# Kernel optimization log

Hardware: AMD Instinct MI355X
Metric: run time of the kernel (lower is better)

The kernel has to match this reference:

```python
import jax, jax.numpy as jnp
from jax import lax
import numpy as np

B, DIM, HEADS, L, K = 8, 128, 8, 4096, 3
INNER = DIM * HEADS
PAD = K // 2
EPS = 1e-5
SCALE = DIM ** -0.5


def setup_inputs() -> dict:
    key = jax.random.key(0)
    ks = jax.random.split(key, 32)

    def n(i, shape, s):
        return jax.random.normal(ks[i], shape, jnp.float32) * s

    inp = {"x": jax.random.normal(ks[0], (B, DIM, L), jnp.float32)}
    inp["ln1_g"] = jnp.ones((DIM,), jnp.float32)
    inp["ln1_b"] = jnp.zeros((DIM,), jnp.float32)
    for idx, p in enumerate(("q", "k", "v")):
        base = 1 + idx * 2
        inp[p + "_dw"] = n(base, (DIM, 1, K), 0.2)        # depthwise kernel
        inp[p + "_bn_g"] = jnp.ones((DIM,), jnp.float32)
        inp[p + "_bn_b"] = jnp.zeros((DIM,), jnp.float32)
        inp[p + "_bn_m"] = jnp.zeros((DIM,), jnp.float32)  # running mean
        inp[p + "_bn_v"] = jnp.ones((DIM,), jnp.float32)   # running var
        inp[p + "_pw"] = n(base + 1, (INNER, DIM), 0.05)   # 1x1 conv dim->inner
    inp["dwc_dw"] = n(8, (DIM,), 0.2)                      # kernel-1 depthwise = per-channel scale
    inp["dwc_bn_g"] = jnp.ones((DIM,), jnp.float32)
    inp["dwc_bn_b"] = jnp.zeros((DIM,), jnp.float32)
    inp["dwc_bn_m"] = jnp.zeros((DIM,), jnp.float32)
    inp["dwc_bn_v"] = jnp.ones((DIM,), jnp.float32)
    inp["dwc_pw"] = n(9, (DIM, DIM), 0.05)
    inp["out_w"] = n(10, (DIM, INNER), 0.05)
    inp["out_b"] = jnp.zeros((DIM,), jnp.float32)
    inp["ln2_g"] = jnp.ones((DIM,), jnp.float32)
    inp["ln2_b"] = jnp.zeros((DIM,), jnp.float32)
    inp["ff_w1"] = n(11, (4 * DIM, DIM), 0.05)
    inp["ff_b1"] = jnp.zeros((4 * DIM,), jnp.float32)
    inp["ff_w2"] = n(12, (DIM, 4 * DIM), 0.05)
    inp["ff_b2"] = jnp.zeros((DIM,), jnp.float32)
    return inp


def _layernorm(x, g, b):
    # channel-wise LN over axis=1 (unbiased=False variance)
    m = jnp.mean(x, axis=1, keepdims=True)
    v = jnp.var(x, axis=1, keepdims=True)
    return (x - m) / jnp.sqrt(v + EPS) * g[None, :, None] + b[None, :, None]


def _dw_block(x, dw, g, b, m, v, pw):
    # depthwise conv (k=K, same padding) -> eval-mode BN -> 1x1 conv
    y = lax.conv_general_dilated(x, dw, (1,), [(PAD, PAD)],
                                 feature_group_count=DIM,
                                 dimension_numbers=("NCH", "OIH", "NCH"))
    y = (y - m[None, :, None]) * (g / jnp.sqrt(v + EPS))[None, :, None] + b[None, :, None]
    return jnp.einsum("oi,bil->bol", pw, y)


def reference(x, ln1_g, ln1_b,
              q_dw, q_bn_g, q_bn_b, q_bn_m, q_bn_v, q_pw,
              k_dw, k_bn_g, k_bn_b, k_bn_m, k_bn_v, k_pw,
              v_dw, v_bn_g, v_bn_b, v_bn_m, v_bn_v, v_pw,
              dwc_dw, dwc_bn_g, dwc_bn_b, dwc_bn_m, dwc_bn_v, dwc_pw,
              out_w, out_b, ln2_g, ln2_b, ff_w1, ff_b1, ff_w2, ff_b2):
    # ---- attention block (PreNorm + residual) ----
    xn = _layernorm(x, ln1_g, ln1_b)
    q = _dw_block(xn, q_dw, q_bn_g, q_bn_b, q_bn_m, q_bn_v, q_pw)  # [B, INNER, L]
    k = _dw_block(xn, k_dw, k_bn_g, k_bn_b, k_bn_m, k_bn_v, k_pw)
    v = _dw_block(xn, v_dw, v_bn_g, v_bn_b, v_bn_m, v_bn_v, v_pw)

    def split(t):  # b (h d) x -> (b h) x d
        return t.reshape(B, HEADS, DIM, L).transpose(0, 1, 3, 2).reshape(B * HEADS, L, DIM)

    q, k, v = split(q), split(k), split(v)
    k_soft = jax.nn.softmax(k, axis=-1)                       # softmax over feature dim d
    kk = jnp.einsum("nxd,nxe->nde", q, k_soft) * SCALE        # [(bh), d, d]
    # DWConv gate on q (kernel-1 depthwise -> BN -> 1x1), channels = DIM
    g_ = q * dwc_dw[None, None, :]
    g_ = (g_ - dwc_bn_m) * (dwc_bn_g / jnp.sqrt(dwc_bn_v + EPS)) + dwc_bn_b
    g_ = jnp.einsum("od,nxd->nxo", dwc_pw, g_)
    gate = jax.nn.sigmoid(g_) * v
    out = jnp.einsum("nxd,nde->nxe", v, kk) + gate            # [(bh), L, d]
    out = out.reshape(B, HEADS, L, DIM).transpose(0, 1, 3, 2).reshape(B, INNER, L)
    attn = jnp.einsum("oi,bil->bol", out_w, out) + out_b[None, :, None]
    x = attn + x

    # ---- feed-forward block (PreNorm + residual) ----
    xn = _layernorm(x, ln2_g, ln2_b)
    h = jnp.einsum("oi,bil->bol", ff_w1, xn) + ff_b1[None, :, None]
    h = jax.nn.gelu(h, approximate=False)
    h = jnp.einsum("oi,bil->bol", ff_w2, h) + ff_b2[None, :, None]
    return h + x
```

## Files before the change

kernel.cpp:

```cpp
#include <hip/hip_runtime.h>
#include <hip/hip_bf16.h>
#include <math.h>

#define DI __device__ __forceinline__

namespace {

constexpr int L = 4096;
constexpr float EPS = 1e-5f;
constexpr float SCALEF = 0.08838834764831845f;

typedef unsigned short u16;
typedef unsigned int u32;
typedef unsigned char u8;
typedef __attribute__((ext_vector_type(8))) short bf16x8;
typedef __attribute__((ext_vector_type(4))) float f32x4;

DI float b2f(u16 h){ u32 u = ((u32)h) << 16; float f; __builtin_memcpy(&f, &u, 4); return f; }
DI u16 f2b(float f){ u32 u; __builtin_memcpy(&u, &f, 4); u32 r = u + 0x7fffu + ((u >> 16) & 1u); return (u16)(r >> 16); }
DI float sigmoidf(float x){ return 1.f / (1.f + __expf(-x)); }

DI uint2 pack_fp8x8(const float* v){
  u32 lo = __builtin_amdgcn_cvt_pk_fp8_f32(v[0], v[1], 0, false);
  lo = (u32)__builtin_amdgcn_cvt_pk_fp8_f32(v[2], v[3], lo, true);
  u32 hi = __builtin_amdgcn_cvt_pk_fp8_f32(v[4], v[5], 0, false);
  hi = (u32)__builtin_amdgcn_cvt_pk_fp8_f32(v[6], v[7], hi, true);
  return make_uint2(lo, hi);
}
DI u8 f2e(float v){ return (u8)__builtin_amdgcn_cvt_pk_fp8_f32(v, v, 0, false); }
DI float e2f(u8 c){ return __builtin_amdgcn_cvt_f32_fp8((int)c, 0); }

DI int boff(int o, int d8){ return ((o >> 4) << 11) + (d8 << 7) + (((o & 15) ^ d8) << 3); }
DI int foff(int g, int k8, int nn){ return (g << 11) + (k8 << 7) + (nn << 3); }
DI int faddr(int x, int e){ return ((x >> 4) << 11) + ((e >> 3) << 7) + ((x & 15) << 3) + (e & 7); }
DI int t8off(int dhi, int nl, int x8){ return (dhi << 11) + (x8 << 7) + (((nl ^ x8 ^ dhi) & 15) << 3); }

DI void stage_a(const u16* __restrict__ g, int rs, u16* a_s, int tid){
  #pragma unroll
  for (int it = 0; it < 4; it++){
    int item = tid + 256 * it;
    int d8 = item & 15, l = item >> 4;
    *(uint4*)&a_s[l * 136 + d8 * 8] = *(const uint4*)&g[(size_t)l * rs + d8 * 8];
  }
}

__global__ __launch_bounds__(256) void ln_kernel(
    const float* __restrict__ x, const float* __restrict__ g,
    const float* __restrict__ bt, u16* __restrict__ o)
{
  const int tid = threadIdx.x;
  const int pos = blockIdx.x * 64 + (tid >> 2);
  const int part = tid & 3;
  const int b = pos >> 12, l = pos & (L - 1);
  const float* xb = x + (size_t)b * 128 * L + l;
  float vv[32];
  float s = 0.f, ss = 0.f;
  #pragma unroll
  for (int i = 0; i < 32; i++){
    float v = xb[(size_t)(part * 32 + i) * L];
    vv[i] = v; s += v; ss += v * v;
  }
  s += __shfl_xor(s, 1);  s += __shfl_xor(s, 2);
  ss += __shfl_xor(ss, 1); ss += __shfl_xor(ss, 2);
  const float m = s * (1.f / 128.f);
  const float rs = rsqrtf(ss * (1.f / 128.f) - m * m + EPS);
  #pragma unroll
  for (int c = 0; c < 4; c++){
    u16 pk[8];
    #pragma unroll
    for (int j = 0; j < 8; j++){
      int d = part * 32 + c * 8 + j;
      pk[j] = f2b((vv[c * 8 + j] - m) * rs * g[d] + bt[d]);
    }
    uint4 uu; __builtin_memcpy(&uu, pk, 16);
    *(uint4*)&o[(size_t)pos * 128 + part * 32 + c * 8] = uu;
  }
}

__global__ __launch_bounds__(256) void wpack_kernel(
    const float* __restrict__ q_pw, const float* __restrict__ k_pw,
    const float* __restrict__ v_pw, const float* __restrict__ out_w,
    const float* __restrict__ ff_w1, const float* __restrict__ ff_w2,
    const float* __restrict__ dwc_dw, const float* __restrict__ dwc_bng,
    const float* __restrict__ dwc_bnb, const float* __restrict__ dwc_bnm,
    const float* __restrict__ dwc_bnv, const float* __restrict__ dwc_pw,
    u16* __restrict__ wpk, u8* __restrict__ w2tb8, float* __restrict__ c2,
    u8* __restrict__ wpk8)
{
  const int blk = blockIdx.x;
  if (blk < 320){
    int item = blk * 256 + threadIdx.x;
    int d8 = item & 15;
    int o  = (item >> 4) & 127;
    int t  = item >> 11;
    const float* src;
    if (t < 24){
      int p = t >> 3, h = t & 7;
      const float* pw = (p == 0) ? q_pw : (p == 1 ? k_pw : v_pw);
      src = pw + (size_t)(h * 128 + o) * 128 + d8 * 8;
    } else if (t < 32){
      src = out_w + (size_t)o * 1024 + (t - 24) * 128 + d8 * 8;
    } else if (t < 36){
      src = ff_w1 + (size_t)((t - 32) * 128 + o) * 128 + d8 * 8;
    } else {
      src = ff_w2 + (size_t)o * 512 + (t - 36) * 128 + d8 * 8;
    }
    u16 pk[8];
    #pragma unroll
    for (int j = 0; j < 8; j++) pk[j] = f2b(src[j]);
    uint4 uu; __builtin_memcpy(&uu, pk, 16);
    *(uint4*)&wpk[(size_t)t * 16384 + boff(o, d8)] = uu;
  } else if (blk == 320){
    #pragma unroll
    for (int it = 0; it < 8; it++){
      int item = threadIdx.x + 256 * it;
      int nn = item & 15, k8 = (item >> 4) & 15, os = item >> 8;
      int e = os * 16 + nn;
      float fv[8];
      #pragma unroll
      for (int j = 0; j < 8; j++){
        int d = k8 * 8 + j;
        float sD = dwc_bng[d] * rsqrtf(dwc_bnv[d] + EPS);
        fv[j] = dwc_pw[(size_t)e * 128 + d] * dwc_dw[d] * sD * 16.f;
      }
      *(uint2*)&w2tb8[foff(os, k8, nn)] = pack_fp8x8(fv);
    }
  } else if (blk == 321){
    int e = threadIdx.x;
    if (e < 128){
      float cacc = 0.f;
      for (int d = 0; d < 128; d++){
        float sD = dwc_bng[d] * rsqrtf(dwc_bnv[d] + EPS);
        cacc += dwc_pw[(size_t)e * 128 + d] * (dwc_bnb[d] - dwc_bnm[d] * sD);
      }
      c2[e] = cacc;
    }
  } else {
    int h = blk - 322;
    #pragma unroll
    for (int it = 0; it < 8; it++){
      int item = threadIdx.x + 256 * it;
      int nn = item & 15, k8 = (item >> 4) & 15, os = item >> 8;
      int o = os * 16 + nn;
      float fv[8];
      #pragma unroll
      for (int j = 0; j < 8; j++)
        fv[j] = out_w[(size_t)o * 1024 + h * 128 + k8 * 8 + j] * 16.f;
      *(uint2*)&wpk8[(h << 14) + foff(os, k8, nn)] = pack_fp8x8(fv);
    }
  }
}

struct QkvArgs {
  const float* dw[3];
  const float* bng[3];
  const float* bnb[3];
  const float* bnm[3];
  const float* bnv[3];
  u8* outp[3];
};

__global__ __launch_bounds__(256, 3) void qkv_fused_kernel(
    const u16* __restrict__ xnb, const u16* __restrict__ wpk, QkvArgs args)
{
  __shared__ u16 y_s[64 * 136];
  __shared__ u16 w_s[128 * 128];
  __shared__ float4 coef[128];
  const int tid = threadIdx.x;
  const int lb = blockIdx.x;
  const int oh = blockIdx.y;
  const int bz = blockIdx.z;
  const int b  = bz / 3;
  const int p  = bz % 3;
  const int l0 = lb * 64;
  const int lane = tid & 63, wv = tid >> 6;
  const int nn = lane & 15, quad = lane >> 4;
  const int d8s = tid & 15;

  if (tid < 128){
    int d = tid;
    float sD = args.bng[p][d] * rsqrtf(args.bnv[p][d] + EPS);
    const float* dw = args.dw[p];
    coef[d] = make_float4(dw[d * 3] * sD, dw[d * 3 + 1] * sD, dw[d * 3 + 2] * sD,
                          args.bnb[p][d] - args.bnm[p][d] * sD);
  }
  __syncthreads();
  float4 cf[8];
  #pragma unroll
  for (int jj = 0; jj < 8; jj++) cf[jj] = coef[d8s * 8 + jj];
  #pragma unroll
  for (int it = 0; it < 4; it++){
    int l = (tid >> 4) + it * 16;
    int gl = l0 + l;
    const u16* rowp = xnb + ((size_t)b * L + gl) * 128 + d8s * 8;
    uint4 uc = *(const uint4*)rowp;
    uint4 um = (gl > 0)     ? *(const uint4*)(rowp - 128) : make_uint4(0, 0, 0, 0);
    uint4 up = (gl < L - 1) ? *(const uint4*)(rowp + 128) : make_uint4(0, 0, 0, 0);
    u16 em[8], ec[8], ep[8];
    __builtin_memcpy(em, &um, 16); __builtin_memcpy(ec, &uc, 16); __builtin_memcpy(ep, &up, 16);
    u16 pk[8];
    #pragma unroll
    for (int jj = 0; jj < 8; jj++)
      pk[jj] = f2b(cf[jj].x * b2f(em[jj]) + cf[jj].y * b2f(ec[jj]) + cf[jj].z * b2f(ep[jj]) + cf[jj].w);
    uint4 uu; __builtin_memcpy(&uu, pk, 16);
    *(uint4*)&y_s[l * 136 + d8s * 8] = uu;
  }
  __syncthreads();
  bf16x8 af[4];
  #pragma unroll
  for (int dc = 0; dc < 4; dc++)
    af[dc] = *(const bf16x8*)&y_s[(wv * 16 + nn) * 136 + ((dc << 2) + quad) * 8];

  for (int hh = 0; hh < 4; hh++){
    const int h = oh * 4 + hh;
    const int ph = p * 8 + h;
    if (hh) __syncthreads();
    const u16* src = wpk + ((size_t)ph << 14);
    #pragma unroll
    for (int it = 0; it < 8; it++){
      int idx = (tid + 256 * it) << 3;
      *(uint4*)&w_s[idx] = *(const uint4*)&src[idx];
    }
    __syncthreads();
    f32x4 acc[8];
    #pragma unroll
    for (int os = 0; os < 8; os++) acc[os] = (f32x4){0.f, 0.f, 0.f, 0.f};
    #pragma unroll
    for (int os = 0; os < 8; os++){
      #pragma unroll
      for (int dc = 0; dc < 4; dc++){
        int d8 = (dc << 2) + quad;
        bf16x8 bf = *(const bf16x8*)&w_s[(os << 11) + (d8 << 7) + ((nn ^ d8) << 3)];
        acc[os] = __builtin_amdgcn_mfma_f32_16x16x32_bf16(af[dc], bf, acc[os], 0, 0, 0);
      }
    }
    if (p == 1){
      #pragma unroll
      for (int r = 0; r < 4; r++){
        float m = acc[0][r];
        #pragma unroll
        for (int os = 1; os < 8; os++) m = fmaxf(m, acc[os][r]);
        m = fmaxf(m, __shfl_xor(m, 1));
        m = fmaxf(m, __shfl_xor(m, 2));
        m = fmaxf(m, __shfl_xor(m, 4));
        m = fmaxf(m, __shfl_xor(m, 8));
        float s = 0.f;
        #pragma unroll
        for (int os = 0; os < 8; os++){ acc[os][r] = __expf(acc[os][r] - m); s += acc[os][r]; }
        s += __shfl_xor(s, 1);
        s += __shfl_xor(s, 2);
        s += __shfl_xor(s, 4);
        s += __shfl_xor(s, 8);
        float inv = 16.f / s;
        #pragma unroll
        for (int os = 0; os < 8; os++) acc[os][r] *= inv;
      }
    }
    __syncthreads();
    u16* st = w_s;
    #pragma unroll
    for (int os = 0; os < 8; os++)
      #pragma unroll
      for (int r = 0; r < 4; r++)
        st[(wv * 16 + quad * 4 + r) * 136 + (os << 4) + nn] = f2b(acc[os][r]);
    __syncthreads();
    if (p == 2){
      u8* v8 = args.outp[2];
      size_t tbase = ((size_t)((b * 8 + h) * 64 + lb)) << 13;
      #pragma unroll
      for (int it = 0; it < 4; it++){
        int g = it, e8 = tid >> 4, n2 = tid & 15;
        const u16* sp = &st[(g * 16 + n2) * 136 + e8 * 8];
        float fv[8];
        #pragma unroll
        for (int j = 0; j < 8; j++) fv[j] = b2f(sp[j]);
        *(uint2*)&v8[tbase + foff(g, e8, n2)] = pack_fp8x8(fv);
      }
    } else {
      u8* outp8 = args.outp[p];
      size_t gbase = ((size_t)(b * 8 + h) * L + l0) * 128;
      #pragma unroll
      for (int it = 0; it < 4; it++){
        int item = tid + 256 * it;
        int row = item >> 4, d8 = item & 15;
        const u16* sp = &st[row * 136 + d8 * 8];
        float fv[8];
        #pragma unroll
        for (int j = 0; j < 8; j++) fv[j] = b2f(sp[j]);
        *(uint2*)&outp8[gbase + (size_t)row * 128 + d8 * 8] = pack_fp8x8(fv);
      }
    }
  }
}

__global__ __launch_bounds__(256, 3) void kk_kernel(
    const u8* __restrict__ qt8, const u8* __restrict__ kt8,
    float* __restrict__ kkp)
{
  __shared__ u8 qT8[16384];
  __shared__ u8 kT8[16384];
  const int tid = threadIdx.x;
  const int sp = blockIdx.x;
  const int n  = blockIdx.y;
  const int d8 = tid & 15;
  const int x8 = tid >> 4;
  const int lane = tid & 63, wv = tid >> 6;
  const int nn = lane & 15, quad = lane >> 4;
  const int m4 = (wv >> 1) << 2;
  const int e4 = (wv & 1) << 2;
  const size_t gbase = ((size_t)n * L + sp * 1024) * 128;

  uint2 rq[8], rk[8];
  #pragma unroll
  for (int j = 0; j < 8; j++){
    size_t off = gbase + (size_t)(x8 * 8 + j) * 128 + d8 * 8;
    rq[j] = *(const uint2*)&qt8[off];
    rk[j] = *(const uint2*)&kt8[off];
  }

  f32x4 acc[4][4];
  #pragma unroll
  for (int mi = 0; mi < 4; mi++)
    #pragma unroll
    for (int ei = 0; ei < 4; ei++) acc[mi][ei] = (f32x4){0.f, 0.f, 0.f, 0.f};

  for (int c = 0; c < 8; c++){
    #pragma unroll
    for (int i = 0; i < 8; i++){
      u8 cq[8], ck[8];
      #pragma unroll
      for (int j = 0; j < 8; j++){
        u8 tmp[8];
        __builtin_memcpy(tmp, &rq[j], 8); cq[j] = tmp[i];
        __builtin_memcpy(tmp, &rk[j], 8); ck[j] = tmp[i];
      }
      int d = d8 * 8 + i;
      int off = t8off(d >> 4, d & 15, x8);
      uint2 uq, uk;
      __builtin_memcpy(&uq, cq, 8); __builtin_memcpy(&uk, ck, 8);
      *(uint2*)&qT8[off] = uq;
      *(uint2*)&kT8[off] = uk;
    }
    __syncthreads();
    if (c < 7){
      #pragma unroll
      for (int j = 0; j < 8; j++){
        size_t off = gbase + (size_t)((c + 1) * 128 + x8 * 8 + j) * 128 + d8 * 8;
        rq[j] = *(const uint2*)&qt8[off];
        rk[j] = *(const uint2*)&kt8[off];
      }
    }
    #pragma unroll
    for (int ks = 0; ks < 4; ks++){
      int x8f = (ks << 2) + quad;
      long af[4], bf[4];
      #pragma unroll
      for (int t = 0; t < 4; t++){
        af[t] = *(const long*)&qT8[t8off(m4 + t, nn, x8f)];
        bf[t] = *(const long*)&kT8[t8off(e4 + t, nn, x8f)];
      }
      #pragma unroll
      for (int mi = 0; mi < 4; mi++)
        #pragma unroll
        for (int ei = 0; ei < 4; ei++)
          acc[mi][ei] = __builtin_amdgcn_mfma_f32_16x16x32_fp8_fp8(af[mi], bf[ei], acc[mi][ei], 0, 0, 0);
    }
    __syncthreads();
  }

  float* op = kkp + ((size_t)(sp * 64 + n) << 14);
  #pragma unroll
  for (int mi = 0; mi < 4; mi++){
    #pragma unroll
    for (int r = 0; r < 4; r++){
      int d = (m4 << 4) + mi * 16 + quad * 4 + r;
      #pragma unroll
      for (int ei = 0; ei < 4; ei++)
        op[d * 128 + (e4 << 4) + ei * 16 + nn] = acc[mi][ei][r];
    }
  }
}

__global__ __launch_bounds__(256) void kkred_kernel(
    const float* __restrict__ kkp, u8* __restrict__ kkbb8)
{
  int item = blockIdx.x * 256 + threadIdx.x;
  int nn = item & 15, d8 = (item >> 4) & 15, os = (item >> 8) & 7, n = item >> 11;
  int e = os * 16 + nn;
  float fv[8];
  #pragma unroll
  for (int j = 0; j < 8; j++){
    float s = 0.f;
    #pragma unroll
    for (int sp = 0; sp < 4; sp++)
      s += kkp[(size_t)sp * (64 * 16384) + n * 16384 + (d8 * 8 + j) * 128 + e];
    fv[j] = s * (SCALEF * 2.f);
  }
  *(uint2*)&kkbb8[((size_t)n << 14) + foff(os, d8, nn)] = pack_fp8x8(fv);
}

__global__ __launch_bounds__(256, 4) void gateout_kernel(
    const u8* __restrict__ qt8, const u8* __restrict__ vt8,
    const u8* __restrict__ kkbb8, const u8* __restrict__ w2tb8,
    const float* __restrict__ c2, u8* __restrict__ outt8)
{
  __shared__ __attribute__((aligned(16))) u8 q_s8[64 * 144];
  __shared__ __attribute__((aligned(16))) u8 v_s8[8192];
  const int tid = threadIdx.x;
  const int lb = blockIdx.x;
  const int n  = blockIdx.y;
  const int l0 = lb * 64;
  const int lane = tid & 63, wv = tid >> 6;
  const int nn = lane & 15, quad = lane >> 4;
  const size_t vtile = ((size_t)(n * 64 + lb)) << 13;
  const size_t qbase = ((size_t)n * L + l0) * 128;

  #pragma unroll
  for (int it = 0; it < 4; it++){
    int item = tid + 256 * it;
    int d8b = item & 15, l = item >> 4;
    *(uint2*)&q_s8[l * 144 + d8b * 8] = *(const uint2*)&qt8[qbase + (size_t)l * 128 + d8b * 8];
  }
  #pragma unroll
  for (int it = 0; it < 2; it++){
    int idx = (tid + 256 * it) << 4;
    *(uint4*)&v_s8[idx] = *(const uint4*)&vt8[vtile + idx];
  }
  __syncthreads();

  long aq[4], av[4];
  #pragma unroll
  for (int dc = 0; dc < 4; dc++){
    aq[dc] = *(const long*)&q_s8[(wv * 16 + nn) * 144 + ((dc << 2) + quad) * 8];
    av[dc] = *(const long*)&v_s8[foff(wv, (dc << 2) + quad, nn)];
  }
  const u8* kb8 = kkbb8 + ((size_t)n << 14);
  f32x4 acc_o[8], acc_g[8];
  #pragma unroll
  for (int os = 0; os < 8; os++){ acc_o[os] = (f32x4){0,0,0,0}; acc_g[os] = (f32x4){0,0,0,0}; }
  #pragma unroll
  for (int os = 0; os < 8; os++){
    #pragma unroll
    for (int dc = 0; dc < 4; dc++){
      int d8 = (dc << 2) + quad;
      long bkk = *(const long*)&kb8[foff(os, d8, nn)];
      long bw8 = *(const long*)&w2tb8[foff(os, d8, nn)];
      acc_o[os] = __builtin_amdgcn_mfma_f32_16x16x32_fp8_fp8(av[dc], bkk, acc_o[os], 0, 0, 0);
      acc_g[os] = __builtin_amdgcn_mfma_f32_16x16x32_fp8_fp8(aq[dc], bw8, acc_g[os], 0, 0, 0);
    }
  }
  __syncthreads();
  u8* st8 = q_s8;
  #pragma unroll
  for (int os = 0; os < 8; os++){
    int e = (os << 4) + nn;
    float c2v = c2[e];
    #pragma unroll
    for (int r = 0; r < 4; r++){
      int xr = wv * 16 + quad * 4 + r;
      float ve = e2f(v_s8[faddr(xr, e)]);
      float val = acc_o[os][r] * (1.f / 32.f) + sigmoidf(acc_g[os][r] * 0.0625f + c2v) * ve;
      st8[faddr(xr, e)] = f2e(val);
    }
  }
  __syncthreads();
  #pragma unroll
  for (int it = 0; it < 2; it++){
    int idx = (tid + 256 * it) << 4;
    *(uint4*)&outt8[vtile + idx] = *(const uint4*)&st8[idx];
  }
}

__global__ __launch_bounds__(256, 4) void outw_kernel(
    const u8* __restrict__ outt8, const u8* __restrict__ wpk8,
    const float* __restrict__ out_b, const float* __restrict__ x,
    const float* __restrict__ g2, const float* __restrict__ bt2,
    float* __restrict__ x2, u16* __restrict__ xn2b)
{
  __shared__ float stf[128 * 68];
  const int tid = threadIdx.x;
  const int lb = blockIdx.x;
  const int b  = blockIdx.y;
  const int l0 = lb * 64;
  const int lane = tid & 63, wv = tid >> 6;
  const int nn = lane & 15, quad = lane >> 4;
  f32x4 acc[8];
  #pragma unroll
  for (int os = 0; os < 8; os++) acc[os] = (f32x4){0,0,0,0};

  for (int h = 0; h < 8; h++){
    const size_t tbase = ((size_t)((b * 8 + h) * 64 + lb)) << 13;
    long af[4];
    #pragma unroll
    for (int dc = 0; dc < 4; dc++)
      af[dc] = *(const long*)&outt8[tbase + foff(wv, (dc << 2) + quad, nn)];
    const u8* bp8 = wpk8 + (h << 14);
    #pragma unroll
    for (int os = 0; os < 8; os++){
      #pragma unroll
      for (int dc = 0; dc < 4; dc++){
        long bf8 = *(const long*)&bp8[foff(os, (dc << 2) + quad, nn)];
        acc[os] = __builtin_amdgcn_mfma_f32_16x16x32_fp8_fp8(af[dc], bf8, acc[os], 0, 0, 0);
      }
    }
  }
  #pragma unroll
  for (int os = 0; os < 8; os++)
    #pragma unroll
    for (int r = 0; r < 4; r++)
      stf[((os << 4) + nn) * 68 + wv * 16 + quad * 4 + r] = acc[os][r] * 0.0625f;
  __syncthreads();
  {
    int o = tid >> 1, lh = tid & 1;
    float bias = out_b[o];
    size_t gbase = ((size_t)b * 128 + o) * L + l0 + lh * 32;
    float* sp = &stf[o * 68 + lh * 32];
    #pragma unroll
    for (int k = 0; k < 8; k++){
      float4 xv = *(const float4*)&x[gbase + k * 4];
      float4 sv = *(float4*)&sp[k * 4];
      float4 ov = make_float4(sv.x + bias + xv.x, sv.y + bias + xv.y,
                              sv.z + bias + xv.z, sv.w + bias + xv.w);
      *(float4*)&sp[k * 4] = ov;
      *(float4*)&x2[gbase + k * 4] = ov;
    }
  }
  __syncthreads();
  {
    int l = tid >> 2, part = tid & 3;
    float vv[32];
    float s = 0.f, ss = 0.f;
    #pragma unroll
    for (int i = 0; i < 32; i++){
      float v = stf[(part * 32 + i) * 68 + l];
      vv[i] = v; s += v; ss += v * v;
    }
    s += __shfl_xor(s, 1);  s += __shfl_xor(s, 2);
    ss += __shfl_xor(ss, 1); ss += __shfl_xor(ss, 2);
    float m = s * (1.f / 128.f);
    float rs = rsqrtf(ss * (1.f / 128.f) - m * m + EPS);
    #pragma unroll
    for (int c = 0; c < 4; c++){
      u16 pk[8];
      #pragma unroll
      for (int j = 0; j < 8; j++){
        int d = part * 32 + c * 8 + j;
        pk[j] = f2b((vv[c * 8 + j] - m) * rs * g2[d] + bt2[d]);
      }
      uint4 uu; __builtin_memcpy(&uu, pk, 16);
      *(uint4*)&xn2b[((size_t)b * L + l0 + l) * 128 + part * 32 + c * 8] = uu;
    }
  }
}

__global__ __launch_bounds__(256, 2) void ff_fused_kernel(
    const u16* __restrict__ xn2b, const u16* __restrict__ wpk,
    const float* __restrict__ b1, const float* __restrict__ b2,
    const float* __restrict__ x2, float* __restrict__ outp)
{
  __shared__ u16 a_s[64 * 136];
  __shared__ u16 h_s[64 * 136];
  const int tid = threadIdx.x;
  const int lb = blockIdx.x;
  const int b  = blockIdx.y;
  const int l0 = lb * 64;
  const int lane = tid & 63, wv = tid >> 6;
  const int nn = lane & 15, quad = lane >> 4;

  stage_a(xn2b + ((size_t)b * L + l0) * 128, 128, a_s, tid);
  __syncthreads();
  bf16x8 af[4];
  #pragma unroll
  for (int dc = 0; dc < 4; dc++)
    af[dc] = *(const bf16x8*)&a_s[(wv * 16 + nn) * 136 + ((dc << 2) + quad) * 8];

  f32x4 acc_out[8];
  #pragma unroll
  for (int os = 0; os < 8; os++) acc_out[os] = (f32x4){0.f, 0.f, 0.f, 0.f};

  for (int fc = 0; fc < 4; fc++){
    const u16* bp1 = wpk + (size_t)(32 + fc) * 16384;
    f32x4 hacc[8];
    #pragma unroll
    for (int os = 0; os < 8; os++) hacc[os] = (f32x4){0.f, 0.f, 0.f, 0.f};
    #pragma unroll
    for (int os = 0; os < 8; os++){
      #pragma unroll
      for (int dc = 0; dc < 4; dc++){
        int d8 = (dc << 2) + quad;
        bf16x8 bf = *(const bf16x8*)&bp1[(os << 11) + (d8 << 7) + ((nn ^ d8) << 3)];
        hacc[os] = __builtin_amdgcn_mfma_f32_16x16x32_bf16(af[dc], bf, hacc[os], 0, 0, 0);
      }
    }
    __syncthreads();
    #pragma unroll
    for (int os = 0; os < 8; os++){
      float bias = b1[fc * 128 + (os << 4) + nn];
      #pragma unroll
      for (int r = 0; r < 4; r++){
        float v = hacc[os][r] + bias;
        float ge = 0.5f * v * (1.f + erff(v * 0.70710678118654752f));
        h_s[(wv * 16 + quad * 4 + r) * 136 + (os << 4) + nn] = f2b(ge);
      }
    }
    __syncthreads();
    bf16x8 hf[4];
    #pragma unroll
    for (int dc = 0; dc < 4; dc++)
      hf[dc] = *(const bf16x8*)&h_s[(wv * 16 + nn) * 136 + ((dc << 2) + quad) * 8];
    const u16* bp2 = wpk + (size_t)(36 + fc) * 16384;
    #pragma unroll
    for (int os = 0; os < 8; os++){
      #pragma unroll
      for (int dc = 0; dc < 4; dc++){
        int d8 = (dc << 2) + quad;
        bf16x8 bf = *(const bf16x8*)&bp2[(os << 11) + (d8 << 7) + ((nn ^ d8) << 3)];
        acc_out[os] = __builtin_amdgcn_mfma_f32_16x16x32_bf16(hf[dc], bf, acc_out[os], 0, 0, 0);
      }
    }
  }

  float* stf = (float*)h_s;
  #pragma unroll
  for (int t = 0; t < 2; t++){
    __syncthreads();
    #pragma unroll
    for (int osl = 0; osl < 4; osl++){
      int os = t * 4 + osl;
      #pragma unroll
      for (int r = 0; r < 4; r++)
        stf[((osl << 4) + nn) * 68 + wv * 16 + quad * 4 + r] = acc_out[os][r];
    }
    __syncthreads();
    int ol = tid >> 2;
    int o  = t * 64 + ol;
    int lc = (tid & 3) * 16;
    float bias = b2[o];
    size_t gbase = ((size_t)b * 128 + o) * L + l0 + lc;
    #pragma unroll
    for (int k = 0; k < 4; k++){
      float4 sv = *(const float4*)&stf[ol * 68 + lc + k * 4];
      float4 xv = *(const float4*)&x2[gbase + k * 4];
      *(float4*)&outp[gbase + k * 4] = make_float4(sv.x + bias + xv.x, sv.y + bias + xv.y,
                                                   sv.z + bias + xv.z, sv.w + bias + xv.w);
    }
  }
}

}

extern "C" void kernel_launch(void* const* d_in, const int* in_sizes, int n_in,
                              void* d_out, int out_size, void* d_ws, size_t ws_size,
                              hipStream_t stream)
{
  const float* x      = (const float*)d_in[0];
  const float* ln1_g  = (const float*)d_in[1];
  const float* ln1_b  = (const float*)d_in[2];
  const float* q_dw   = (const float*)d_in[3];
  const float* q_bng  = (const float*)d_in[4];
  const float* q_bnb  = (const float*)d_in[5];
  const float* q_bnm  = (const float*)d_in[6];
  const float* q_bnv  = (const float*)d_in[7];
  const float* q_pw   = (const float*)d_in[8];
  const float* k_dw   = (const float*)d_in[9];
  const float* k_bng  = (const float*)d_in[10];
  const float* k_bnb  = (const float*)d_in[11];
  const float* k_bnm  = (const float*)d_in[12];
  const float* k_bnv  = (const float*)d_in[13];
  const float* k_pw   = (const float*)d_in[14];
  const float* v_dw   = (const float*)d_in[15];
  const float* v_bng  = (const float*)d_in[16];
  const float* v_bnb  = (const float*)d_in[17];
  const float* v_bnm  = (const float*)d_in[18];
  const float* v_bnv  = (const float*)d_in[19];
  const float* v_pw   = (const float*)d_in[20];
  const float* dwc_dw  = (const float*)d_in[21];
  const float* dwc_bng = (const float*)d_in[22];
  const float* dwc_bnb = (const float*)d_in[23];
  const float* dwc_bnm = (const float*)d_in[24];
  const float* dwc_bnv = (const float*)d_in[25];
  const float* dwc_pw  = (const float*)d_in[26];
  const float* out_w  = (const float*)d_in[27];
  const float* out_b  = (const float*)d_in[28];
  const float* ln2_g  = (const float*)d_in[29];
  const float* ln2_b  = (const float*)d_in[30];
  const float* ff_w1  = (const float*)d_in[31];
  const float* ff_b1  = (const float*)d_in[32];
  const float* ff_w2  = (const float*)d_in[33];
  const float* ff_b2  = (const float*)d_in[34];
  float* out = (float*)d_out;

  char* w = (char*)d_ws;
  u8*   qt8   = (u8*)(w);
  u8*   kt8   = (u8*)(w + (32ull  << 20));
  u8*   outt8 = (u8*)(w + (64ull  << 20));
  u8*   vt8   = (u8*)(w + (128ull << 20));
  u16*  xnb   = (u16*)(w + (192ull << 20));
  u8*   kkbb8 = (u8*)(w + (192ull << 20));
  u16*  xn2b  = (u16*)(w + (192ull << 20));
  float* kkp  = (float*)(w + (200ull << 20));
  float* x2   = kkp;
  u8*   w2tb8 = (u8*)(w + (216ull << 20));
  float* c2   = (float*)(w + (216ull << 20) + 16384);
  u16*  wpk   = (u16*)(w + (216ull << 20) + 65536);
  u8*   wpk8  = (u8*)(w + (218ull << 20));

  ln_kernel<<<512, 256, 0, stream>>>(x, ln1_g, ln1_b, xnb);
  wpack_kernel<<<330, 256, 0, stream>>>(q_pw, k_pw, v_pw, out_w, ff_w1, ff_w2,
                                        dwc_dw, dwc_bng, dwc_bnb, dwc_bnm, dwc_bnv, dwc_pw,
                                        wpk, w2tb8, c2, wpk8);

  QkvArgs qa;
  qa.dw[0] = q_dw;  qa.bng[0] = q_bng; qa.bnb[0] = q_bnb; qa.bnm[0] = q_bnm; qa.bnv[0] = q_bnv; qa.outp[0] = qt8;
  qa.dw[1] = k_dw;  qa.bng[1] = k_bng; qa.bnb[1] = k_bnb; qa.bnm[1] = k_bnm; qa.bnv[1] = k_bnv; qa.outp[1] = kt8;
  qa.dw[2] = v_dw;  qa.bng[2] = v_bng; qa.bnb[2] = v_bnb; qa.bnm[2] = v_bnm; qa.bnv[2] = v_bnv; qa.outp[2] = vt8;
  qkv_fused_kernel<<<dim3(64, 2, 24), 256, 0, stream>>>(xnb, wpk, qa);

  kk_kernel<<<dim3(4, 64), 256, 0, stream>>>(qt8, kt8, kkp);
  kkred_kernel<<<512, 256, 0, stream>>>(kkp, kkbb8);
  gateout_kernel<<<dim3(64, 64), 256, 0, stream>>>(qt8, vt8, kkbb8, w2tb8, c2, outt8);
  outw_kernel<<<dim3(64, 8), 256, 0, stream>>>(outt8, wpk8, out_b, x, ln2_g, ln2_b, x2, xn2b);

  ff_fused_kernel<<<dim3(64, 8), 256, 0, stream>>>(xn2b, wpk, ff_b1, ff_b2, x2, out);
}
```

Measured before the change: 383.3 us.

## Switch QKV projection and FF first GEMM to FP8 MFMA with unified FP8 weight pack

Converts the QKV pointwise projections and the first feed-forward GEMM from bf16 to fp8 MFMA. Activations (the depthwise-conv output and the LN2 output) are quantized to fp8, and the weights are prepacked as fp8 scaled by 16, with results rescaled by 1/16. The weight-pack kernel is restructured to emit one contiguous fp8 weight buffer, which also holds the out-projection and gate weights. Only ff_w2 stays in bf16. This halves operand bytes and LDS traffic and raises the occupancy hints, at the cost of reduced numerical accuracy from fp8 quantization.

```diff
diff --git a/kernel.cpp b/kernel.cpp
--- a/kernel.cpp
+++ b/kernel.cpp
@@ -82,51 +82,57 @@
     const float* __restrict__ v_pw, const float* __restrict__ out_w,
     const float* __restrict__ ff_w1, const float* __restrict__ ff_w2,
     const float* __restrict__ dwc_dw, const float* __restrict__ dwc_bng,
-    const float* __restrict__ dwc_bnb, const float* __restrict__ dwc_bnm,
-    const float* __restrict__ dwc_bnv, const float* __restrict__ dwc_pw,
-    u16* __restrict__ wpk, u8* __restrict__ w2tb8, float* __restrict__ c2,
-    u8* __restrict__ wpk8)
+    const float* __restrict__ dwc_bnv, const float* __restrict__ dwc_bnb,
+    const float* __restrict__ dwc_bnm, const float* __restrict__ dwc_pw,
+    u16* __restrict__ wpk, float* __restrict__ c2, u8* __restrict__ wpk8)
 {
   const int blk = blockIdx.x;
-  if (blk < 320){
-    int item = blk * 256 + threadIdx.x;
-    int d8 = item & 15;
-    int o  = (item >> 4) & 127;
-    int t  = item >> 11;
-    const float* src;
-    if (t < 24){
-      int p = t >> 3, h = t & 7;
-      const float* pw = (p == 0) ? q_pw : (p == 1 ? k_pw : v_pw);
-      src = pw + (size_t)(h * 128 + o) * 128 + d8 * 8;
-    } else if (t < 32){
-      src = out_w + (size_t)o * 1024 + (t - 24) * 128 + d8 * 8;
-    } else if (t < 36){
-      src = ff_w1 + (size_t)((t - 32) * 128 + o) * 128 + d8 * 8;
-    } else {
-      src = ff_w2 + (size_t)o * 512 + (t - 36) * 128 + d8 * 8;
-    }
+  const int tid = threadIdx.x;
+  if (blk < 37){
+    int t8 = blk;
+    #pragma unroll
+    for (int it = 0; it < 8; it++){
+      int item = tid + 256 * it;
+      int nn = item & 15, k8 = (item >> 4) & 15, os = item >> 8;
+      int o = os * 16 + nn;
+      float fv[8];
+      if (t8 < 24){
+        int p = t8 >> 3, h = t8 & 7;
+        const float* pw = (p == 0) ? q_pw : (p == 1 ? k_pw : v_pw);
+        #pragma unroll
+        for (int j = 0; j < 8; j++)
+          fv[j] = pw[(size_t)(h * 128 + o) * 128 + k8 * 8 + j] * 16.f;
+      } else if (t8 < 32){
+        #pragma unroll
+        for (int j = 0; j < 8; j++)
+          fv[j] = out_w[(size_t)o * 1024 + (t8 - 24) * 128 + k8 * 8 + j] * 16.f;
+      } else if (t8 < 36){
+        #pragma unroll
+        for (int j = 0; j < 8; j++)
+          fv[j] = ff_w1[(size_t)((t8 - 32) * 128 + o) * 128 + k8 * 8 + j] * 16.f;
+      } else {
+        #pragma unroll
+        for (int j = 0; j < 8; j++){
+          int d = k8 * 8 + j;
+          float sD = dwc_bng[d] * rsqrtf(dwc_bnv[d] + EPS);
+          fv[j] = dwc_pw[(size_t)o * 128 + d] * dwc_dw[d] * sD * 16.f;
+        }
+      }
+      *(uint2*)&wpk8[(size_t)t8 * 16384 + foff(os, k8, nn)] = pack_fp8x8(fv);
+    }
+  } else if (blk < 69){
+    int vitem = (blk - 37) * 256 + tid;
+    int d8 = vitem & 15;
+    int o  = (vitem >> 4) & 127;
+    int t  = 36 + (vitem >> 11);
+    const float* src = ff_w2 + (size_t)o * 512 + (t - 36) * 128 + d8 * 8;
     u16 pk[8];
     #pragma unroll
     for (int j = 0; j < 8; j++) pk[j] = f2b(src[j]);
     uint4 uu; __builtin_memcpy(&uu, pk, 16);
     *(uint4*)&wpk[(size_t)t * 16384 + boff(o, d8)] = uu;
-  } else if (blk == 320){
-    #pragma unroll
-    for (int it = 0; it < 8; it++){
-      int item = threadIdx.x + 256 * it;
-      int nn = item & 15, k8 = (item >> 4) & 15, os = item >> 8;
-      int e = os * 16 + nn;
-      float fv[8];
-      #pragma unroll
-      for (int j = 0; j < 8; j++){
-        int d = k8 * 8 + j;
-        float sD = dwc_bng[d] * rsqrtf(dwc_bnv[d] + EPS);
-        fv[j] = dwc_pw[(size_t)e * 128 + d] * dwc_dw[d] * sD * 16.f;
-      }
-      *(uint2*)&w2tb8[foff(os, k8, nn)] = pack_fp8x8(fv);
-    }
-  } else if (blk == 321){
-    int e = threadIdx.x;
+  } else {
+    int e = tid;
     if (e < 128){
       float cacc = 0.f;
       for (int d = 0; d < 128; d++){
@@ -134,19 +140,6 @@
         cacc += dwc_pw[(size_t)e * 128 + d] * (dwc_bnb[d] - dwc_bnm[d] * sD);
       }
       c2[e] = cacc;
-    }
-  } else {
-    int h = blk - 322;
-    #pragma unroll
-    for (int it = 0; it < 8; it++){
-      int item = threadIdx.x + 256 * it;
-      int nn = item & 15, k8 = (item >> 4) & 15, os = item >> 8;
-      int o = os * 16 + nn;
-      float fv[8];
-      #pragma unroll
-      for (int j = 0; j < 8; j++)
-        fv[j] = out_w[(size_t)o * 1024 + h * 128 + k8 * 8 + j] * 16.f;
-      *(uint2*)&wpk8[(h << 14) + foff(os, k8, nn)] = pack_fp8x8(fv);
     }
   }
 }
@@ -160,11 +153,11 @@
   u8* outp[3];
 };
 
-__global__ __launch_bounds__(256, 3) void qkv_fused_kernel(
-    const u16* __restrict__ xnb, const u16* __restrict__ wpk, QkvArgs args)
-{
-  __shared__ u16 y_s[64 * 136];
-  __shared__ u16 w_s[128 * 128];
+__global__ __launch_bounds__(256, 5) void qkv_fused_kernel(
+    const u16* __restrict__ xnb, const u8* __restrict__ wpk8, QkvArgs args)
+{
+  __shared__ __attribute__((aligned(16))) u8 y_s8[64 * 136];
+  __shared__ u16 st_s[64 * 136];
   __shared__ float4 coef[128];
   const int tid = threadIdx.x;
   const int lb = blockIdx.x;
@@ -176,6 +169,7 @@
   const int lane = tid & 63, wv = tid >> 6;
   const int nn = lane & 15, quad = lane >> 4;
   const int d8s = tid & 15;
+  u8* w_s8 = (u8*)st_s;
 
   if (tid < 128){
     int d = tid;
@@ -198,28 +192,26 @@
     uint4 up = (gl < L - 1) ? *(const uint4*)(rowp + 128) : make_uint4(0, 0, 0, 0);
     u16 em[8], ec[8], ep[8];
     __builtin_memcpy(em, &um, 16); __builtin_memcpy(ec, &uc, 16); __builtin_memcpy(ep, &up, 16);
-    u16 pk[8];
+    float fv[8];
     #pragma unroll
     for (int jj = 0; jj < 8; jj++)
-      pk[jj] = f2b(cf[jj].x * b2f(em[jj]) + cf[jj].y * b2f(ec[jj]) + cf[jj].z * b2f(ep[jj]) + cf[jj].w);
-    uint4 uu; __builtin_memcpy(&uu, pk, 16);
-    *(uint4*)&y_s[l * 136 + d8s * 8] = uu;
+      fv[jj] = cf[jj].x * b2f(em[jj]) + cf[jj].y * b2f(ec[jj]) + cf[jj].z * b2f(ep[jj]) + cf[jj].w;
+    *(uint2*)&y_s8[l * 136 + d8s * 8] = pack_fp8x8(fv);
   }
   __syncthreads();
-  bf16x8 af[4];
+  long afq[4];
   #pragma unroll
   for (int dc = 0; dc < 4; dc++)
-    af[dc] = *(const bf16x8*)&y_s[(wv * 16 + nn) * 136 + ((dc << 2) + quad) * 8];
+    afq[dc] = *(const long*)&y_s8[(wv * 16 + nn) * 136 + ((dc << 2) + quad) * 8];
 
   for (int hh = 0; hh < 4; hh++){
     const int h = oh * 4 + hh;
-    const int ph = p * 8 + h;
     if (hh) __syncthreads();
-    const u16* src = wpk + ((size_t)ph << 14);
-    #pragma unroll
-    for (int it = 0; it < 8; it++){
-      int idx = (tid + 256 * it) << 3;
-      *(uint4*)&w_s[idx] = *(const uint4*)&src[idx];
+    const u8* src = wpk8 + ((size_t)(p * 8 + h) << 14);
+    #pragma unroll
+    for (int it = 0; it < 4; it++){
+      int idx = (tid + 256 * it) << 4;
+      *(uint4*)&w_s8[idx] = *(const uint4*)&src[idx];
     }
     __syncthreads();
     f32x4 acc[8];
@@ -230,10 +222,14 @@
       #pragma unroll
       for (int dc = 0; dc < 4; dc++){
         int d8 = (dc << 2) + quad;
-        bf16x8 bf = *(const bf16x8*)&w_s[(os << 11) + (d8 << 7) + ((nn ^ d8) << 3)];
-        acc[os] = __builtin_amdgcn_mfma_f32_16x16x32_bf16(af[dc], bf, acc[os], 0, 0, 0);
-      }
-    }
+        long bf8 = *(const long*)&w_s8[foff(os, d8, nn)];
+        acc[os] = __builtin_amdgcn_mfma_f32_16x16x32_fp8_fp8(afq[dc], bf8, acc[os], 0, 0, 0);
+      }
+    }
+    #pragma unroll
+    for (int os = 0; os < 8; os++)
+      #pragma unroll
+      for (int r = 0; r < 4; r++) acc[os][r] *= 0.0625f;
     if (p == 1){
       #pragma unroll
       for (int r = 0; r < 4; r++){
@@ -257,12 +253,11 @@
       }
     }
     __syncthreads();
-    u16* st = w_s;
     #pragma unroll
     for (int os = 0; os < 8; os++)
       #pragma unroll
       for (int r = 0; r < 4; r++)
-        st[(wv * 16 + quad * 4 + r) * 136 + (os << 4) + nn] = f2b(acc[os][r]);
+        st_s[(wv * 16 + quad * 4 + r) * 136 + (os << 4) + nn] = f2b(acc[os][r]);
     __syncthreads();
     if (p == 2){
       u8* v8 = args.outp[2];
@@ -270,7 +265,7 @@
       #pragma unroll
       for (int it = 0; it < 4; it++){
         int g = it, e8 = tid >> 4, n2 = tid & 15;
-        const u16* sp = &st[(g * 16 + n2) * 136 + e8 * 8];
+        const u16* sp = &st_s[(g * 16 + n2) * 136 + e8 * 8];
         float fv[8];
         #pragma unroll
         for (int j = 0; j < 8; j++) fv[j] = b2f(sp[j]);
@@ -283,7 +278,7 @@
       for (int it = 0; it < 4; it++){
         int item = tid + 256 * it;
         int row = item >> 4, d8 = item & 15;
-        const u16* sp = &st[row * 136 + d8 * 8];
+        const u16* sp = &st_s[row * 136 + d8 * 8];
         float fv[8];
         #pragma unroll
         for (int j = 0; j < 8; j++) fv[j] = b2f(sp[j]);
@@ -472,10 +467,10 @@
 }
 
 __global__ __launch_bounds__(256, 4) void outw_kernel(
-    const u8* __restrict__ outt8, const u8* __restrict__ wpk8,
+    const u8* __restrict__ outt8, const u8* __restrict__ wpk8o,
     const float* __restrict__ out_b, const float* __restrict__ x,
     const float* __restrict__ g2, const float* __restrict__ bt2,
-    float* __restrict__ x2, u16* __restrict__ xn2b)
+    float* __restrict__ x2, u8* __restrict__ xn2b8)
 {
   __shared__ float stf[128 * 68];
   const int tid = threadIdx.x;
@@ -494,7 +489,7 @@
     #pragma unroll
     for (int dc = 0; dc < 4; dc++)
       af[dc] = *(const long*)&outt8[tbase + foff(wv, (dc << 2) + quad, nn)];
-    const u8* bp8 = wpk8 + (h << 14);
+    const u8* bp8 = wpk8o + (h << 14);
     #pragma unroll
     for (int os = 0; os < 8; os++){
       #pragma unroll
@@ -541,24 +536,24 @@
     float rs = rsqrtf(ss * (1.f / 128.f) - m * m + EPS);
     #pragma unroll
     for (int c = 0; c < 4; c++){
-      u16 pk[8];
+      float fv[8];
       #pragma unroll
       for (int j = 0; j < 8; j++){
         int d = part * 32 + c * 8 + j;
-        pk[j] = f2b((vv[c * 8 + j] - m) * rs * g2[d] + bt2[d]);
-      }
-      uint4 uu; __builtin_memcpy(&uu, pk, 16);
-      *(uint4*)&xn2b[((size_t)b * L + l0 + l) * 128 + part * 32 + c * 8] = uu;
-    }
-  }
-}
-
-__global__ __launch_bounds__(256, 2) void ff_fused_kernel(
-    const u16* __restrict__ xn2b, const u16* __restrict__ wpk,
+        fv[j] = (vv[c * 8 + j] - m) * rs * g2[d] + bt2[d];
+      }
+      *(uint2*)&xn2b8[((size_t)b * L + l0 + l) * 128 + part * 32 + c * 8] = pack_fp8x8(fv);
+    }
+  }
+}
+
+__global__ __launch_bounds__(256, 4) void ff_fused_kernel(
+    const u8* __restrict__ xn2b8, const u8* __restrict__ wpk8,
+    const u16* __restrict__ wpk,
     const float* __restrict__ b1, const float* __restrict__ b2,
     const float* __restrict__ x2, float* __restrict__ outp)
 {
-  __shared__ u16 a_s[64 * 136];
+  __shared__ __attribute__((aligned(16))) u8 a_s8[64 * 136];
   __shared__ u16 h_s[64 * 136];
   const int tid = threadIdx.x;
   const int lb = blockIdx.x;
@@ -567,19 +562,25 @@
   const int lane = tid & 63, wv = tid >> 6;
   const int nn = lane & 15, quad = lane >> 4;
 
-  stage_a(xn2b + ((size_t)b * L + l0) * 128, 128, a_s, tid);
+  #pragma unroll
+  for (int it = 0; it < 4; it++){
+    int item = tid + 256 * it;
+    int d8 = item & 15, l = item >> 4;
+    *(uint2*)&a_s8[l * 136 + d8 * 8] =
+        *(const uint2*)&xn2b8[((size_t)b * L + l0 + l) * 128 + d8 * 8];
+  }
   __syncthreads();
-  bf16x8 af[4];
+  long af8[4];
   #pragma unroll
   for (int dc = 0; dc < 4; dc++)
-    af[dc] = *(const bf16x8*)&a_s[(wv * 16 + nn) * 136 + ((dc << 2) + quad) * 8];
+    af8[dc] = *(const long*)&a_s8[(wv * 16 + nn) * 136 + ((dc << 2) + quad) * 8];
 
   f32x4 acc_out[8];
   #pragma unroll
   for (int os = 0; os < 8; os++) acc_out[os] = (f32x4){0.f, 0.f, 0.f, 0.f};
 
   for (int fc = 0; fc < 4; fc++){
-    const u16* bp1 = wpk + (size_t)(32 + fc) * 16384;
+    const u8* bp1 = wpk8 + (size_t)(32 + fc) * 16384;
     f32x4 hacc[8];
     #pragma unroll
     for (int os = 0; os < 8; os++) hacc[os] = (f32x4){0.f, 0.f, 0.f, 0.f};
@@ -587,9 +588,8 @@
     for (int os = 0; os < 8; os++){
       #pragma unroll
       for (int dc = 0; dc < 4; dc++){
-        int d8 = (dc << 2) + quad;
-        bf16x8 bf = *(const bf16x8*)&bp1[(os << 11) + (d8 << 7) + ((nn ^ d8) << 3)];
-        hacc[os] = __builtin_amdgcn_mfma_f32_16x16x32_bf16(af[dc], bf, hacc[os], 0, 0, 0);
+        long bf8 = *(const long*)&bp1[foff(os, (dc << 2) + quad, nn)];
+        hacc[os] = __builtin_amdgcn_mfma_f32_16x16x32_fp8_fp8(af8[dc], bf8, hacc[os], 0, 0, 0);
       }
     }
     __syncthreads();
@@ -598,7 +598,7 @@
       float bias = b1[fc * 128 + (os << 4) + nn];
       #pragma unroll
       for (int r = 0; r < 4; r++){
-        float v = hacc[os][r] + bias;
+        float v = hacc[os][r] * 0.0625f + bias;
         float ge = 0.5f * v * (1.f + erff(v * 0.70710678118654752f));
         h_s[(wv * 16 + quad * 4 + r) * 136 + (os << 4) + nn] = f2b(ge);
       }
@@ -697,29 +697,30 @@
   u8*   vt8   = (u8*)(w + (128ull << 20));
   u16*  xnb   = (u16*)(w + (192ull << 20));
   u8*   kkbb8 = (u8*)(w + (192ull << 20));
-  u16*  xn2b  = (u16*)(w + (192ull << 20));
+  u8*   xn2b8 = (u8*)(w + (192ull << 20));
   float* kkp  = (float*)(w + (200ull << 20));
   float* x2   = kkp;
-  u8*   w2tb8 = (u8*)(w + (216ull << 20));
-  float* c2   = (float*)(w + (216ull << 20) + 16384);
+  float* c2   = (float*)(w + (216ull << 20));
   u16*  wpk   = (u16*)(w + (216ull << 20) + 65536);
   u8*   wpk8  = (u8*)(w + (218ull << 20));
+  u8*   wpk8o = wpk8 + ((size_t)24 << 14);
+  u8*   w2tb8 = wpk8 + ((size_t)36 << 14);
 
   ln_kernel<<<512, 256, 0, stream>>>(x, ln1_g, ln1_b, xnb);
-  wpack_kernel<<<330, 256, 0, stream>>>(q_pw, k_pw, v_pw, out_w, ff_w1, ff_w2,
-                                        dwc_dw, dwc_bng, dwc_bnb, dwc_bnm, dwc_bnv, dwc_pw,
-                                        wpk, w2tb8, c2, wpk8);
+  wpack_kernel<<<70, 256, 0, stream>>>(q_pw, k_pw, v_pw, out_w, ff_w1, ff_w2,
+                                       dwc_dw, dwc_bng, dwc_bnv, dwc_bnb, dwc_bnm, dwc_pw,
+                                       wpk, c2, wpk8);
 
   QkvArgs qa;
   qa.dw[0] = q_dw;  qa.bng[0] = q_bng; qa.bnb[0] = q_bnb; qa.bnm[0] = q_bnm; qa.bnv[0] = q_bnv; qa.outp[0] = qt8;
   qa.dw[1] = k_dw;  qa.bng[1] = k_bng; qa.bnb[1] = k_bnb; qa.bnm[1] = k_bnm; qa.bnv[1] = k_bnv; qa.outp[1] = kt8;
   qa.dw[2] = v_dw;  qa.bng[2] = v_bng; qa.bnb[2] = v_bnb; qa.bnm[2] = v_bnm; qa.bnv[2] = v_bnv; qa.outp[2] = vt8;
-  qkv_fused_kernel<<<dim3(64, 2, 24), 256, 0, stream>>>(xnb, wpk, qa);
+  qkv_fused_kernel<<<dim3(64, 2, 24), 256, 0, stream>>>(xnb, wpk8, qa);
 
   kk_kernel<<<dim3(4, 64), 256, 0, stream>>>(qt8, kt8, kkp);
   kkred_kernel<<<512, 256, 0, stream>>>(kkp, kkbb8);
   gateout_kernel<<<dim3(64, 64), 256, 0, stream>>>(qt8, vt8, kkbb8, w2tb8, c2, outt8);
-  outw_kernel<<<dim3(64, 8), 256, 0, stream>>>(outt8, wpk8, out_b, x, ln2_g, ln2_b, x2, xn2b);
-
-  ff_fused_kernel<<<dim3(64, 8), 256, 0, stream>>>(xn2b, wpk, ff_b1, ff_b2, x2, out);
-}
+  outw_kernel<<<dim3(64, 8), 256, 0, stream>>>(outt8, wpk8o, out_b, x, ln2_g, ln2_b, x2, xn2b8);
+
+  ff_fused_kernel<<<dim3(64, 8), 256, 0, stream>>>(xn2b8, wpk8, wpk, ff_b1, ff_b2, x2, out);
+}
```

Result: faster. 354.8 us (-7.4%).
